# Kernel tuning notes

Measured on AMD Instinct MI355X. Metric: run time of the kernel, lower is better.

Reference implementation:

```python
import jax, jax.numpy as jnp
import numpy as np

B = 8192       # Monte Carlo paths
NSTEP = 30     # Euler time steps
D = 100        # z_dim / number of assets
H1 = 110
H2 = 110
T = NSTEP - 1  # number of subnets
DT = np.float32(1.0 / NSTEP)
R = np.float32(0.05)   # riskfree
EPS = np.float32(1e-3) # Keras BatchNormalization epsilon


def setup_inputs() -> dict:
    key = jax.random.key(0)
    ks = jax.random.split(key, 25)
    f = jnp.float32
    X = jax.random.normal(ks[0], (B, NSTEP, D), f)
    DWs = jax.random.normal(ks[1], (B, NSTEP, D), f) * jnp.sqrt(DT)
    sigmas = jax.random.uniform(ks[2], (D,), f, 0.1, 0.4)
    y_init = jax.random.uniform(ks[3], (1,), f, 0.0, 1.0)
    z_init = jax.random.uniform(ks[4], (1, D), f, -0.1, 0.1)
    W1 = jax.random.normal(ks[5], (T, D, H1), f) / np.sqrt(D).astype(np.float32)
    W2 = jax.random.normal(ks[6], (T, H1, H2), f) / np.sqrt(H1).astype(np.float32)
    W3 = jax.random.normal(ks[7], (T, H2, D), f) / np.sqrt(H2).astype(np.float32)
    dims = [D, H1, H2, D]
    bn = {}
    for j, dim in enumerate(dims):
        bn[f"g{j}"] = 1.0 + 0.1 * jax.random.normal(ks[8 + 4 * j], (T, dim), f)
        bn[f"b{j}"] = 0.05 * jax.random.normal(ks[9 + 4 * j], (T, dim), f)
        bn[f"m{j}"] = 0.1 * jax.random.normal(ks[10 + 4 * j], (T, dim), f)
        bn[f"v{j}"] = jax.random.uniform(ks[11 + 4 * j], (T, dim), f, 0.5, 1.5)
    return dict(X=X, DWs=DWs, sigmas=sigmas, y_init=y_init, z_init=z_init,
                W1=W1, W2=W2, W3=W3, **bn)


def _bn(x, g, b, m, v):
    # Keras BatchNormalization, inference mode
    return (x - m) * jax.lax.rsqrt(v + EPS) * g + b


def _subnet(x, p):
    (w1, w2, w3, g0, b0, m0, v0, g1, b1, m1, v1,
     g2, b2, m2, v2, g3, b3, m3, v3) = p
    x = _bn(x, g0, b0, m0, v0)
    x = jax.nn.relu(x @ w1)
    x = _bn(x, g1, b1, m1, v1)
    x = jax.nn.relu(x @ w2)
    x = _bn(x, g2, b2, m2, v2)
    x = x @ w3
    return _bn(x, g3, b3, m3, v3)


def reference(X, DWs, sigmas, y_init, z_init, W1, W2, W3,
              g0, b0, m0, v0, g1, b1, m1, v1,
              g2, b2, m2, v2, g3, b3, m3, v3):
    nb = X.shape[0]
    Y0 = jnp.ones((nb, 1), X.dtype) * y_init            # [B,1]
    Z0 = jnp.ones((nb, 1), X.dtype) * z_init            # [B,D]

    def step(carry, xs):
        Y, Z = carry
        Xi, Xn, DWi, p = xs
        Y = Y + R * Y * DT + jnp.sum(sigmas * Xi * Z * DWi, axis=1, keepdims=True)
        Z = _subnet(Xn, p)
        return (Y, Z), None

    params = (W1, W2, W3, g0, b0, m0, v0, g1, b1, m1, v1,
              g2, b2, m2, v2, g3, b3, m3, v3)  # each leading dim T
    xs = (jnp.moveaxis(X[:, :T], 1, 0),        # [T,B,D]
          jnp.moveaxis(X[:, 1:T + 1], 1, 0),   # [T,B,D]
          jnp.moveaxis(DWs[:, :T], 1, 0),      # [T,B,D]
          params)
    (Y, Z), _ = jax.lax.scan(step, (Y0, Z0), xs)
    # final step: X[:,-2,:] with DWs[:,-1,:]
    Y = Y + R * Y * DT + jnp.sum(sigmas * X[:, -2, :] * Z * DWs[:, -1, :],
                                 axis=1, keepdims=True)
    return Y
```

## Files before the change

### kernel.cpp

```cpp
#include <hip/hip_runtime.h>

typedef unsigned short ushort_t;
typedef __attribute__((ext_vector_type(8))) short s16x8;
typedef __attribute__((ext_vector_type(4))) float f32x4;

#define B_PATHS 8192
#define NSTEP   30
#define DD      100
#define HH      110
#define TT      29
#define ROWSTR  3000
#define LDK     136
#define WFRAGSZ 14336
#define DT_C    (1.0f/30.0f)
#define R_C     0.05f
#define EPS_C   1e-3f

__device__ __forceinline__ ushort_t f2bf(float f) {
  unsigned u = __float_as_uint(f);
  u = u + 0x7FFFu + ((u >> 16) & 1u);
  return (ushort_t)(u >> 16);
}
__device__ __forceinline__ float bf2f(ushort_t u) {
  return __uint_as_float(((unsigned)u) << 16);
}

__global__ void prep_kernel(const float* __restrict__ W1, const float* __restrict__ W2,
                            const float* __restrict__ W3,
                            const float* g0, const float* b0, const float* m0, const float* v0,
                            const float* g1, const float* b1, const float* m1, const float* v1,
                            const float* g2, const float* b2, const float* m2, const float* v2,
                            const float* g3, const float* b3, const float* m3, const float* v3,
                            ushort_t* __restrict__ wprep, float* __restrict__ bprep)
{
  const int mat = blockIdx.x, t = blockIdx.y, tid = threadIdx.x;
  __shared__ float wsh[110*110];
  __shared__ float sin_[112], hin_[112], sout_[112], hout_[112];

  int Kr, Nr; const float* W; const float *g, *bb, *mm, *vv;
  if (mat == 0)      { Kr = 100; Nr = 110; W = W1 + t*11000; g = g0+t*100; bb = b0+t*100; mm = m0+t*100; vv = v0+t*100; }
  else if (mat == 1) { Kr = 110; Nr = 110; W = W2 + t*12100; g = g1+t*110; bb = b1+t*110; mm = m1+t*110; vv = v1+t*110; }
  else               { Kr = 110; Nr = 100; W = W3 + t*11000; g = g2+t*110; bb = b2+t*110; mm = m2+t*110; vv = v2+t*110; }

  if (tid < Kr) {
    float s = g[tid] * rsqrtf(vv[tid] + EPS_C);
    sin_[tid] = s; hin_[tid] = bb[tid] - mm[tid]*s;
  }
  if (mat == 2 && tid < Nr) {
    float s = g3[t*100+tid] * rsqrtf(v3[t*100+tid] + EPS_C);
    sout_[tid] = s; hout_[tid] = b3[t*100+tid] - m3[t*100+tid]*s;
  }
  for (int i = tid; i < Kr*Nr; i += 256) wsh[i] = W[i];
  __syncthreads();

  if (tid < 128) {
    float c = 0.f;
    if (tid < Nr) {
      for (int k = 0; k < Kr; ++k) c += hin_[k] * wsh[k*Nr + tid];
      if (mat == 2) c = c * sout_[tid] + hout_[tid];
    }
    bprep[(t*3 + mat)*128 + tid] = c;
  }

  ushort_t* wo = wprep + (size_t)(t*3 + mat) * WFRAGSZ;
  for (int ch = tid; ch < 1792; ch += 256) {
    const int lane = ch & 63, ntkb = ch >> 6;
    const int nt = ntkb % 7, kb = ntkb / 7;
    const int n  = nt*16 + (lane & 15);
    const int k0 = kb*32 + (lane >> 4)*8;
    ushort_t tmp[8];
#pragma unroll
    for (int j = 0; j < 8; ++j) {
      const int k = k0 + j;
      float v = 0.f;
      if (n < Nr && k < Kr) {
        v = sin_[k] * wsh[k*Nr + n];
        if (mat == 2) v *= sout_[n];
      }
      tmp[j] = f2bf(v);
    }
    ushort4 lo; lo.x = tmp[0]; lo.y = tmp[1]; lo.z = tmp[2]; lo.w = tmp[3];
    ushort4 hi; hi.x = tmp[4]; hi.y = tmp[5]; hi.z = tmp[6]; hi.w = tmp[7];
    *(ushort4*)(wo + ch*8)     = lo;
    *(ushort4*)(wo + ch*8 + 4) = hi;
  }
}

__device__ __forceinline__ void mlp_stage32(ushort_t* act, const ushort_t* __restrict__ wfrag,
                                            const float* __restrict__ biasg,
                                            int wrow, int lane, int lrow, int quad, bool relu)
{
  f32x4 acc[7][2];
  const f32x4 z4 = {0.f, 0.f, 0.f, 0.f};
#pragma unroll
  for (int nt = 0; nt < 7; ++nt) { acc[nt][0] = z4; acc[nt][1] = z4; }

#pragma unroll
  for (int kb = 0; kb < 4; ++kb) {
    const s16x8 a0 = *(const s16x8*)(act + (wrow      + lrow)*LDK + kb*32 + quad*8);
    const s16x8 a1 = *(const s16x8*)(act + (wrow + 16 + lrow)*LDK + kb*32 + quad*8);
    s16x8 b[7];
#pragma unroll
    for (int nt = 0; nt < 7; ++nt)
      b[nt] = *(const s16x8*)(wfrag + ((kb*7 + nt)*64 + lane)*8);
#pragma unroll
    for (int nt = 0; nt < 7; ++nt) {
      acc[nt][0] = __builtin_amdgcn_mfma_f32_16x16x32_bf16(a0, b[nt], acc[nt][0], 0, 0, 0);
      acc[nt][1] = __builtin_amdgcn_mfma_f32_16x16x32_bf16(a1, b[nt], acc[nt][1], 0, 0, 0);
    }
  }

#pragma unroll
  for (int nt = 0; nt < 7; ++nt) {
    const int col = nt*16 + lrow;
    const float bv = biasg[col];
#pragma unroll
    for (int mh = 0; mh < 2; ++mh) {
#pragma unroll
      for (int r = 0; r < 4; ++r) {
        float u = acc[nt][mh][r] + bv;
        if (relu) u = u > 0.f ? u : 0.f;
        act[(wrow + mh*16 + quad*4 + r)*LDK + col] = f2bf(u);
      }
    }
  }
#pragma unroll
  for (int mh = 0; mh < 2; ++mh)
#pragma unroll
    for (int r = 0; r < 4; ++r)
      act[(wrow + mh*16 + quad*4 + r)*LDK + 112 + lrow] = 0;
}

__global__ __launch_bounds__(128, 4)
void subnet_kernel(const float* __restrict__ X, const float* __restrict__ DW,
                   const float* __restrict__ sigmas,
                   const ushort_t* __restrict__ wprep, const float* __restrict__ bprep,
                   float* __restrict__ sbuf)
{
  __shared__ __align__(16) ushort_t act[64*LDK];

  const int tid  = threadIdx.x;
  const int t    = blockIdx.y;
  const int m0   = blockIdx.x * 64;
  const int lane = tid & 63;
  const int wrow = (tid >> 6) * 32;
  const int lrow = lane & 15, quad = lane >> 4;

  {
    const int c  = lane & 31;
    const int r0 = lane >> 5;
#pragma unroll
    for (int i = 0; i < 16; ++i) {
      const int r = r0 + i*2;
      ushort4 u; u.x = 0; u.y = 0; u.z = 0; u.w = 0;
      if (c < 25) {
        const float4 v = *(const float4*)(X + (size_t)(m0 + wrow + r)*ROWSTR + (t+1)*DD + c*4);
        u.x = f2bf(v.x); u.y = f2bf(v.y); u.z = f2bf(v.z); u.w = f2bf(v.w);
      }
      *(ushort4*)(act + (wrow + r)*LDK + c*4) = u;
    }
  }

  const ushort_t* wf = wprep + (size_t)(t*3) * WFRAGSZ;
  const float*    bg = bprep + (t*3) * 128;

  mlp_stage32(act, wf,             bg,       wrow, lane, lrow, quad, true);
  mlp_stage32(act, wf + WFRAGSZ,   bg + 128, wrow, lane, lrow, quad, true);
  mlp_stage32(act, wf + 2*WFRAGSZ, bg + 256, wrow, lane, lrow, quad, false);

  {
    const int row  = wrow + (lane >> 1);
    const int part = lane & 1;
    const int b    = m0 + row;
    const int xt   = (t == TT - 1) ? (NSTEP - 2) : (t + 1);
    const float* xr = X  + (size_t)b*ROWSTR + xt*DD;
    const float* dr = DW + (size_t)b*ROWSTR + (t+1)*DD;
    float p = 0.f;
#pragma unroll
    for (int g = part; g < 25; g += 2) {
      const float4 xv = *(const float4*)(xr + g*4);
      const float4 dv = *(const float4*)(dr + g*4);
      const float4 sg = *(const float4*)(sigmas + g*4);
      const ushort4 zu = *(const ushort4*)(act + row*LDK + g*4);
      p += sg.x*xv.x*dv.x*bf2f(zu.x);
      p += sg.y*xv.y*dv.y*bf2f(zu.y);
      p += sg.z*xv.z*dv.z*bf2f(zu.z);
      p += sg.w*xv.w*dv.w*bf2f(zu.w);
    }
    p += __shfl_xor(p, 1, 64);
    if (part == 0)
      sbuf[(size_t)(t+1)*B_PATHS + b] = p;
  }
}

__global__ __launch_bounds__(256)
void y_kernel(const float* __restrict__ X, const float* __restrict__ DW,
              const float* __restrict__ sigmas, const float* __restrict__ y_init,
              const float* __restrict__ z_init, const float* __restrict__ sbuf,
              float* __restrict__ out)
{
  const int tid  = threadIdx.x;
  const int row  = tid >> 2, part = tid & 3;
  const int b    = blockIdx.x * 64 + row;
  const float* xr = X + (size_t)b * ROWSTR;
  const float* dr = DW + (size_t)b * ROWSTR;
  float p = 0.f;
#pragma unroll
  for (int g = part; g < 25; g += 4) {
    const float4 xv = *(const float4*)(xr + g*4);
    const float4 dv = *(const float4*)(dr + g*4);
    const float4 sg = *(const float4*)(sigmas + g*4);
    const float4 zv = *(const float4*)(z_init + g*4);
    p += sg.x*xv.x*zv.x*dv.x;
    p += sg.y*xv.y*zv.y*dv.y;
    p += sg.z*xv.z*zv.z*dv.z;
    p += sg.w*xv.w*zv.w*dv.w;
  }
  p += __shfl_xor(p, 1, 64);
  p += __shfl_xor(p, 2, 64);
  if (part == 0) {
    float y = y_init[0];
    y = y + R_C*y*DT_C + p;
#pragma unroll
    for (int tau = 1; tau < NSTEP; ++tau)
      y = y + R_C*y*DT_C + sbuf[(size_t)tau*B_PATHS + b];
    out[b] = y;
  }
}

extern "C" void kernel_launch(void* const* d_in, const int* in_sizes, int n_in,
                              void* d_out, int out_size, void* d_ws, size_t ws_size,
                              hipStream_t stream) {
  const float* X      = (const float*)d_in[0];
  const float* DWs    = (const float*)d_in[1];
  const float* sigmas = (const float*)d_in[2];
  const float* y_init = (const float*)d_in[3];
  const float* z_init = (const float*)d_in[4];
  const float* W1     = (const float*)d_in[5];
  const float* W2     = (const float*)d_in[6];
  const float* W3     = (const float*)d_in[7];
  const float* bn[16];
  for (int i = 0; i < 16; ++i) bn[i] = (const float*)d_in[8 + i];

  char* ws = (char*)d_ws;
  ushort_t* wprep = (ushort_t*)ws;
  float*    bprep = (float*)(ws + 2494464);
  float*    sbuf  = (float*)(ws + 2539008);
  float*    out   = (float*)d_out;

  prep_kernel<<<dim3(3, TT), 256, 0, stream>>>(
      W1, W2, W3,
      bn[0], bn[1], bn[2], bn[3],  bn[4], bn[5], bn[6], bn[7],
      bn[8], bn[9], bn[10], bn[11], bn[12], bn[13], bn[14], bn[15],
      wprep, bprep);
  subnet_kernel<<<dim3(B_PATHS/64, TT), 128, 0, stream>>>(
      X, DWs, sigmas, wprep, bprep, sbuf);
  y_kernel<<<dim3(B_PATHS/64), 256, 0, stream>>>(
      X, DWs, sigmas, y_init, z_init, sbuf, out);
}
```

Before: 348.8 us.

## Halve subnet tile to 16 rows per wave, vectorize weight load, unroll Y recurrence

The subnet kernel now gives each wave 16 rows instead of 32, with half the LDS and accumulator registers per block. The launch bound asks for 8 blocks per CU and the grid doubles, aiming for more occupancy and better latency hiding. The trade is that each block reuses its weight fragments over fewer rows, so weight reads per row double. The prep kernel copies weights with float4 loads, and the Y kernel replaces the serial 30-step recurrence with a closed-form geometric weighted sum spread over 8 lanes, which can change rounding slightly.

```diff
diff --git a/kernel.cpp b/kernel.cpp
--- a/kernel.cpp
+++ b/kernel.cpp
@@ -34,7 +34,7 @@
                             ushort_t* __restrict__ wprep, float* __restrict__ bprep)
 {
   const int mat = blockIdx.x, t = blockIdx.y, tid = threadIdx.x;
-  __shared__ float wsh[110*110];
+  __shared__ __align__(16) float wsh[110*110];
   __shared__ float sin_[112], hin_[112], sout_[112], hout_[112];
 
   int Kr, Nr; const float* W; const float *g, *bb, *mm, *vv;
@@ -50,7 +50,11 @@
     float s = g3[t*100+tid] * rsqrtf(v3[t*100+tid] + EPS_C);
     sout_[tid] = s; hout_[tid] = b3[t*100+tid] - m3[t*100+tid]*s;
   }
-  for (int i = tid; i < Kr*Nr; i += 256) wsh[i] = W[i];
+  {
+    const int n4 = (Kr*Nr) >> 2;
+    for (int i = tid; i < n4; i += 256)
+      ((float4*)wsh)[i] = ((const float4*)W)[i];
+  }
   __syncthreads();
 
   if (tid < 128) {
@@ -86,28 +90,29 @@
   }
 }
 
-__device__ __forceinline__ void mlp_stage32(ushort_t* act, const ushort_t* __restrict__ wfrag,
+__device__ __forceinline__ void mlp_stage16(ushort_t* act, const ushort_t* __restrict__ wfrag,
                                             const float* __restrict__ biasg,
                                             int wrow, int lane, int lrow, int quad, bool relu)
 {
-  f32x4 acc[7][2];
+  f32x4 acc[7];
   const f32x4 z4 = {0.f, 0.f, 0.f, 0.f};
 #pragma unroll
-  for (int nt = 0; nt < 7; ++nt) { acc[nt][0] = z4; acc[nt][1] = z4; }
+  for (int nt = 0; nt < 7; ++nt) acc[nt] = z4;
+
+  s16x8 a[4];
+#pragma unroll
+  for (int kb = 0; kb < 4; ++kb)
+    a[kb] = *(const s16x8*)(act + (wrow + lrow)*LDK + kb*32 + quad*8);
 
 #pragma unroll
   for (int kb = 0; kb < 4; ++kb) {
-    const s16x8 a0 = *(const s16x8*)(act + (wrow      + lrow)*LDK + kb*32 + quad*8);
-    const s16x8 a1 = *(const s16x8*)(act + (wrow + 16 + lrow)*LDK + kb*32 + quad*8);
     s16x8 b[7];
 #pragma unroll
     for (int nt = 0; nt < 7; ++nt)
       b[nt] = *(const s16x8*)(wfrag + ((kb*7 + nt)*64 + lane)*8);
 #pragma unroll
-    for (int nt = 0; nt < 7; ++nt) {
-      acc[nt][0] = __builtin_amdgcn_mfma_f32_16x16x32_bf16(a0, b[nt], acc[nt][0], 0, 0, 0);
-      acc[nt][1] = __builtin_amdgcn_mfma_f32_16x16x32_bf16(a1, b[nt], acc[nt][1], 0, 0, 0);
-    }
+    for (int nt = 0; nt < 7; ++nt)
+      acc[nt] = __builtin_amdgcn_mfma_f32_16x16x32_bf16(a[kb], b[nt], acc[nt], 0, 0, 0);
   }
 
 #pragma unroll
@@ -115,42 +120,37 @@
     const int col = nt*16 + lrow;
     const float bv = biasg[col];
 #pragma unroll
-    for (int mh = 0; mh < 2; ++mh) {
-#pragma unroll
-      for (int r = 0; r < 4; ++r) {
-        float u = acc[nt][mh][r] + bv;
-        if (relu) u = u > 0.f ? u : 0.f;
-        act[(wrow + mh*16 + quad*4 + r)*LDK + col] = f2bf(u);
-      }
-    }
-  }
-#pragma unroll
-  for (int mh = 0; mh < 2; ++mh)
-#pragma unroll
-    for (int r = 0; r < 4; ++r)
-      act[(wrow + mh*16 + quad*4 + r)*LDK + 112 + lrow] = 0;
-}
-
-__global__ __launch_bounds__(128, 4)
+    for (int r = 0; r < 4; ++r) {
+      float u = acc[nt][r] + bv;
+      if (relu) u = u > 0.f ? u : 0.f;
+      act[(wrow + quad*4 + r)*LDK + col] = f2bf(u);
+    }
+  }
+#pragma unroll
+  for (int r = 0; r < 4; ++r)
+    act[(wrow + quad*4 + r)*LDK + 112 + lrow] = 0;
+}
+
+__global__ __launch_bounds__(128, 8)
 void subnet_kernel(const float* __restrict__ X, const float* __restrict__ DW,
                    const float* __restrict__ sigmas,
                    const ushort_t* __restrict__ wprep, const float* __restrict__ bprep,
                    float* __restrict__ sbuf)
 {
-  __shared__ __align__(16) ushort_t act[64*LDK];
+  __shared__ __align__(16) ushort_t act[32*LDK];
 
   const int tid  = threadIdx.x;
   const int t    = blockIdx.y;
-  const int m0   = blockIdx.x * 64;
+  const int m0   = blockIdx.x * 32;
   const int lane = tid & 63;
-  const int wrow = (tid >> 6) * 32;
+  const int wrow = (tid >> 6) * 16;
   const int lrow = lane & 15, quad = lane >> 4;
 
   {
     const int c  = lane & 31;
     const int r0 = lane >> 5;
 #pragma unroll
-    for (int i = 0; i < 16; ++i) {
+    for (int i = 0; i < 8; ++i) {
       const int r = r0 + i*2;
       ushort4 u; u.x = 0; u.y = 0; u.z = 0; u.w = 0;
       if (c < 25) {
@@ -164,20 +164,20 @@
   const ushort_t* wf = wprep + (size_t)(t*3) * WFRAGSZ;
   const float*    bg = bprep + (t*3) * 128;
 
-  mlp_stage32(act, wf,             bg,       wrow, lane, lrow, quad, true);
-  mlp_stage32(act, wf + WFRAGSZ,   bg + 128, wrow, lane, lrow, quad, true);
-  mlp_stage32(act, wf + 2*WFRAGSZ, bg + 256, wrow, lane, lrow, quad, false);
+  mlp_stage16(act, wf,             bg,       wrow, lane, lrow, quad, true);
+  mlp_stage16(act, wf + WFRAGSZ,   bg + 128, wrow, lane, lrow, quad, true);
+  mlp_stage16(act, wf + 2*WFRAGSZ, bg + 256, wrow, lane, lrow, quad, false);
 
   {
-    const int row  = wrow + (lane >> 1);
-    const int part = lane & 1;
+    const int row  = wrow + (lane >> 2);
+    const int part = lane & 3;
     const int b    = m0 + row;
     const int xt   = (t == TT - 1) ? (NSTEP - 2) : (t + 1);
     const float* xr = X  + (size_t)b*ROWSTR + xt*DD;
     const float* dr = DW + (size_t)b*ROWSTR + (t+1)*DD;
     float p = 0.f;
 #pragma unroll
-    for (int g = part; g < 25; g += 2) {
+    for (int g = part; g < 25; g += 4) {
       const float4 xv = *(const float4*)(xr + g*4);
       const float4 dv = *(const float4*)(dr + g*4);
       const float4 sg = *(const float4*)(sigmas + g*4);
@@ -188,6 +188,7 @@
       p += sg.w*xv.w*dv.w*bf2f(zu.w);
     }
     p += __shfl_xor(p, 1, 64);
+    p += __shfl_xor(p, 2, 64);
     if (part == 0)
       sbuf[(size_t)(t+1)*B_PATHS + b] = p;
   }
@@ -200,13 +201,13 @@
               float* __restrict__ out)
 {
   const int tid  = threadIdx.x;
-  const int row  = tid >> 2, part = tid & 3;
-  const int b    = blockIdx.x * 64 + row;
+  const int row  = tid >> 3, part = tid & 7;
+  const int b    = blockIdx.x * 32 + row;
   const float* xr = X + (size_t)b * ROWSTR;
   const float* dr = DW + (size_t)b * ROWSTR;
   float p = 0.f;
 #pragma unroll
-  for (int g = part; g < 25; g += 4) {
+  for (int g = part; g < 25; g += 8) {
     const float4 xv = *(const float4*)(xr + g*4);
     const float4 dv = *(const float4*)(dr + g*4);
     const float4 sg = *(const float4*)(sigmas + g*4);
@@ -218,14 +219,19 @@
   }
   p += __shfl_xor(p, 1, 64);
   p += __shfl_xor(p, 2, 64);
-  if (part == 0) {
-    float y = y_init[0];
-    y = y + R_C*y*DT_C + p;
-#pragma unroll
-    for (int tau = 1; tau < NSTEP; ++tau)
-      y = y + R_C*y*DT_C + sbuf[(size_t)tau*B_PATHS + b];
-    out[b] = y;
-  }
+  p += __shfl_xor(p, 4, 64);
+
+  const float G = 1.f + R_C*DT_C;
+  float ss = 0.f;
+#pragma unroll
+  for (int tau = 1 + part; tau < NSTEP; tau += 8)
+    ss += sbuf[(size_t)tau*B_PATHS + b] * __powf(G, (float)(NSTEP - 1 - tau));
+  ss += __shfl_xor(ss, 1, 64);
+  ss += __shfl_xor(ss, 2, 64);
+  ss += __shfl_xor(ss, 4, 64);
+
+  if (part == 0)
+    out[b] = y_init[0]*__powf(G, 30.f) + p*__powf(G, 29.f) + ss;
 }
 
 extern "C" void kernel_launch(void* const* d_in, const int* in_sizes, int n_in,
@@ -253,8 +259,8 @@
       bn[0], bn[1], bn[2], bn[3],  bn[4], bn[5], bn[6], bn[7],
       bn[8], bn[9], bn[10], bn[11], bn[12], bn[13], bn[14], bn[15],
       wprep, bprep);
-  subnet_kernel<<<dim3(B_PATHS/64, TT), 128, 0, stream>>>(
+  subnet_kernel<<<dim3(B_PATHS/32, TT), 128, 0, stream>>>(
       X, DWs, sigmas, wprep, bprep, sbuf);
-  y_kernel<<<dim3(B_PATHS/64), 256, 0, stream>>>(
+  y_kernel<<<dim3(B_PATHS/32), 256, 0, stream>>>(
       X, DWs, sigmas, y_init, z_init, sbuf, out);
 }
```

Result: no change. 344.3 us (-1.3%).
